# Performance work log

Measured on AMD Instinct MI355X. Metric: run time of the kernel, lower is better.

Reference implementation:

```python
import jax, jax.numpy as jnp
import numpy as np

N_NODES = 100000
N_EDGES = 1600000
NFEAT, NHID, NCLASS, NL = 128, 64, 40, 6


def setup_inputs() -> dict:
    key = jax.random.key(0)
    ks = jax.random.split(key, 12)
    x = jax.random.normal(ks[0], (N_NODES, NFEAT), dtype=jnp.float32)
    edge_row = jax.random.randint(ks[1], (N_EDGES,), 0, N_NODES)
    edge_col = jax.random.randint(ks[2], (N_EDGES,), 0, N_NODES)
    # positive values mimicking a degree-normalized adjacency
    edge_val = jax.random.uniform(ks[3], (N_EDGES,), dtype=jnp.float32) / 16.0
    s1 = 1.0 / np.sqrt(NFEAT)
    sh = 1.0 / np.sqrt(NHID)
    W1 = jax.random.uniform(ks[4], (NFEAT, NHID), minval=-s1, maxval=s1, dtype=jnp.float32)
    b1 = jax.random.uniform(ks[5], (NHID,), minval=-s1, maxval=s1, dtype=jnp.float32)
    Wm = jax.random.uniform(ks[6], (NL, NHID, NHID), minval=-sh, maxval=sh, dtype=jnp.float32)
    bm = jax.random.uniform(ks[7], (NL, NHID), minval=-sh, maxval=sh, dtype=jnp.float32)
    W2 = jax.random.uniform(ks[8], (NHID, NCLASS), minval=-sh, maxval=sh, dtype=jnp.float32)
    b2 = jax.random.uniform(ks[9], (NCLASS,), minval=-sh, maxval=sh, dtype=jnp.float32)
    return {"x": x, "edge_row": edge_row, "edge_col": edge_col, "edge_val": edge_val,
            "W1": W1, "b1": b1, "Wm": Wm, "bm": bm, "W2": W2, "b2": b2}


def _gconv(h, row, col, val, W, b):
    # GraphConvolution: support = h @ W ; out = spmm(adj, support) + b
    support = h @ W                       # [N, out]
    msgs = val[:, None] * support[col]    # [E, out] gather
    agg = jax.ops.segment_sum(msgs, row, num_segments=h.shape[0])  # scatter-add
    return agg + b


def reference(x, edge_row, edge_col, edge_val, W1, b1, Wm, bm, W2, b2):
    # gc1: relu (dropout is identity in eval mode)
    h1 = jax.nn.relu(_gconv(x, edge_row, edge_col, edge_val, W1, b1))
    # first middle layer (module index 2): relu, no residual
    h2 = jax.nn.relu(_gconv(h1, edge_row, edge_col, edge_val, Wm[0], bm[0]))
    prev2, prev = h1, h2
    # remaining middle layers: relu + residual to two layers back
    for k in range(1, NL):
        h = jax.nn.relu(_gconv(prev, edge_row, edge_col, edge_val, Wm[k], bm[k])) + prev2
        prev2, prev = prev, h
    out = _gconv(prev, edge_row, edge_col, edge_val, W2, b2)  # gc2, no relu
    return jax.nn.log_softmax(out, axis=1)
```

## Files before the change

kernel.cpp:

```cpp
#include <hip/hip_runtime.h>
#include <hip/hip_bf16.h>
#include <math.h>

#define N_NODES 100000
#define N_EDGES 1600000
#define NFEAT 128
#define NHID  64
#define NCLASS 40
#define NL 6

#define NBUK 256
#define RPB  391
#define EPP  (N_EDGES / NBUK)
#define EP_PAD 256
#define NTILES (N_NODES / 16)

typedef __attribute__((ext_vector_type(8))) short short8;
typedef __attribute__((ext_vector_type(8))) unsigned short ushort8v;
typedef __attribute__((ext_vector_type(4))) float floatx4;

__device__ __forceinline__ float bfbits(unsigned short u) {
  return __uint_as_float((unsigned int)u << 16);
}
__device__ __forceinline__ short f2bs(float f) {
  __hip_bfloat16 h = __float2bfloat16(f);
  return *reinterpret_cast<short*>(&h);
}

__global__ __launch_bounds__(1024) void p0_hist_k(const int* __restrict__ row,
                                                  int* __restrict__ h2d) {
  __shared__ int h[NBUK];
  const int i = blockIdx.x, t = threadIdx.x;
  if (t < NBUK) h[t] = 0;
  __syncthreads();
  const int e0 = i * EPP, e1 = e0 + EPP;
  for (int e = e0 + t; e < e1; e += 1024) atomicAdd(&h[row[e] / RPB], 1);
  __syncthreads();
  if (t < NBUK) h2d[i * NBUK + t] = h[t];
}

__global__ __launch_bounds__(256) void k1_scanb_k(int* __restrict__ h2d,
                                                  int* __restrict__ btot) {
  __shared__ int sd[256];
  const int b = blockIdx.x, t = threadIdx.x;
  int v = h2d[t * NBUK + b];
  sd[t] = v;
  __syncthreads();
  for (int off = 1; off < 256; off <<= 1) {
    int a = (t >= off) ? sd[t - off] : 0;
    __syncthreads();
    sd[t] += a;
    __syncthreads();
  }
  h2d[t * NBUK + b] = sd[t] - v;
  if (t == 255) btot[b] = sd[255];
}

__global__ __launch_bounds__(256) void k2_scanbase_k(const int* __restrict__ btot,
                                                     int* __restrict__ bbase,
                                                     int2* __restrict__ ep) {
  __shared__ int sd[256];
  const int t = threadIdx.x;
  int v = btot[t];
  sd[t] = v;
  __syncthreads();
  for (int off = 1; off < 256; off <<= 1) {
    int a = (t >= off) ? sd[t - off] : 0;
    __syncthreads();
    sd[t] += a;
    __syncthreads();
  }
  bbase[t] = sd[t] - v;
  if (t == 255) bbase[256] = sd[255];
  if (t < EP_PAD) ep[N_EDGES + t] = make_int2(0, 0);
}

__global__ __launch_bounds__(1024) void p2_part_k(
    const int* __restrict__ row, const int* __restrict__ col,
    const float* __restrict__ val, const int* __restrict__ h2d,
    const int* __restrict__ bbase, int2* __restrict__ pcv,
    unsigned short* __restrict__ plr) {
  __shared__ int cur[NBUK];
  const int i = blockIdx.x, t = threadIdx.x;
  if (t < NBUK) cur[t] = bbase[t] + h2d[i * NBUK + t];
  __syncthreads();
  const int e0 = i * EPP, e1 = e0 + EPP;
  for (int e = e0 + t; e < e1; e += 1024) {
    int r = row[e];
    int b = r / RPB;
    int p = atomicAdd(&cur[b], 1);
    pcv[p] = make_int2(col[e], __float_as_int(val[e]));
    plr[p] = (unsigned short)(r - b * RPB);
  }
}

__global__ __launch_bounds__(1024) void p3_fine_k(const int2* __restrict__ pcv,
                                                  const unsigned short* __restrict__ plr,
                                                  const int* __restrict__ bbase,
                                                  int* __restrict__ rp,
                                                  int2* __restrict__ ep) {
  __shared__ int cnt[RPB];
  __shared__ int cur[RPB];
  const int b = blockIdx.x, t = threadIdx.x;
  const int ebeg = bbase[b], eend = bbase[b + 1];
  const int r0 = b * RPB;
  const int nloc = min(RPB, N_NODES - r0);

  for (int i = t; i < RPB; i += 1024) cnt[i] = 0;
  __syncthreads();
  for (int j = ebeg + t; j < eend; j += 1024) atomicAdd(&cnt[plr[j]], 1);
  __syncthreads();

  if (t < 64) {
    const int base_ = t * 7;
    int v[7], s = 0;
#pragma unroll
    for (int k = 0; k < 7; ++k) {
      int idx = base_ + k;
      v[k] = (idx < RPB) ? cnt[idx] : 0;
      s += v[k];
    }
    int incl = s;
#pragma unroll
    for (int off = 1; off < 64; off <<= 1) {
      int y = __shfl_up(incl, off);
      if (t >= off) incl += y;
    }
    int run = incl - s;
#pragma unroll
    for (int k = 0; k < 7; ++k) {
      int idx = base_ + k;
      if (idx < RPB) cnt[idx] = run;
      run += v[k];
    }
  }
  __syncthreads();

  for (int i = t; i < nloc; i += 1024) {
    rp[r0 + i] = ebeg + cnt[i];
    cur[i] = cnt[i];
  }
  if (b == 0 && t == 0) rp[N_NODES] = N_EDGES;
  __syncthreads();

  for (int j = ebeg + t; j < eend; j += 1024) {
    int lr = plr[j];
    int p = atomicAdd(&cur[lr], 1);
    ep[ebeg + p] = pcv[j];
  }
}

__global__ __launch_bounds__(256) void gemm_l1(const float* __restrict__ X,
                                               const float* __restrict__ W,
                                               unsigned short* __restrict__ S) {
  const int lane = threadIdx.x & 63;
  const int quad = lane >> 4;
  const int m = lane & 15;

  short8 bf[4][4];
#pragma unroll
  for (int t = 0; t < 4; ++t)
#pragma unroll
    for (int h = 0; h < 4; ++h)
#pragma unroll
      for (int j = 0; j < 8; ++j)
        bf[t][h][j] = f2bs(W[(h * 32 + quad * 8 + j) * 64 + t * 16 + m]);

  const int wid = blockIdx.x * 4 + (threadIdx.x >> 6);
  for (int tile = wid; tile < NTILES; tile += gridDim.x * 4) {
    const int r0 = tile * 16;
    const float* xr = X + (size_t)(r0 + m) * 128;
    short8 af[4];
#pragma unroll
    for (int h = 0; h < 4; ++h) {
      const float* p = xr + h * 32 + quad * 8;
      float4 a = *(const float4*)p;
      float4 b = *(const float4*)(p + 4);
      af[h][0] = f2bs(a.x); af[h][1] = f2bs(a.y);
      af[h][2] = f2bs(a.z); af[h][3] = f2bs(a.w);
      af[h][4] = f2bs(b.x); af[h][5] = f2bs(b.y);
      af[h][6] = f2bs(b.z); af[h][7] = f2bs(b.w);
    }
#pragma unroll
    for (int t = 0; t < 4; ++t) {
      floatx4 acc = {0.0f, 0.0f, 0.0f, 0.0f};
#pragma unroll
      for (int h = 0; h < 4; ++h)
        acc = __builtin_amdgcn_mfma_f32_16x16x32_bf16(af[h], bf[t][h], acc, 0, 0, 0);
#pragma unroll
      for (int r = 0; r < 4; ++r)
        S[(size_t)(r0 + quad * 4 + r) * 64 + t * 16 + m] = (unsigned short)f2bs(acc[r]);
    }
  }
}

template <int COLS>
__global__ __launch_bounds__(256) void gemm_bf(const unsigned short* __restrict__ Hb,
                                               const float* __restrict__ W,
                                               unsigned short* __restrict__ S) {
  const int lane = threadIdx.x & 63;
  const int quad = lane >> 4;
  const int m = lane & 15;

  short8 bf[4][2];
#pragma unroll
  for (int t = 0; t < 4; ++t) {
    const int cc = t * 16 + m;
#pragma unroll
    for (int h = 0; h < 2; ++h)
#pragma unroll
      for (int j = 0; j < 8; ++j)
        bf[t][h][j] = (COLS == 64 || cc < COLS)
                          ? f2bs(W[(h * 32 + quad * 8 + j) * COLS + cc])
                          : (short)0;
  }

  const int wid = blockIdx.x * 4 + (threadIdx.x >> 6);
  for (int tile = wid; tile < NTILES; tile += gridDim.x * 4) {
    const int r0 = tile * 16;
    const unsigned short* hr = Hb + (size_t)(r0 + m) * 64 + quad * 8;
    short8 af0 = *(const short8*)hr;
    short8 af1 = *(const short8*)(hr + 32);
#pragma unroll
    for (int t = 0; t < 4; ++t) {
      floatx4 acc = {0.0f, 0.0f, 0.0f, 0.0f};
      acc = __builtin_amdgcn_mfma_f32_16x16x32_bf16(af0, bf[t][0], acc, 0, 0, 0);
      acc = __builtin_amdgcn_mfma_f32_16x16x32_bf16(af1, bf[t][1], acc, 0, 0, 0);
#pragma unroll
      for (int r = 0; r < 4; ++r)
        S[(size_t)(r0 + quad * 4 + r) * 64 + t * 16 + m] = (unsigned short)f2bs(acc[r]);
    }
  }
}

template <bool RES>
__global__ __launch_bounds__(256) void spmm8_k(
    const unsigned short* __restrict__ S, const int2* __restrict__ ep,
    const int* __restrict__ rp, const float* __restrict__ bias,
    unsigned short* __restrict__ Hbout) {
  const int lane = threadIdx.x & 63;
  const int og = lane >> 3;
  const int i8 = lane & 7;
  const int sg = og & 3;
  const bool isB = og >= 4;
  const int pair = blockIdx.x * 4 + (threadIdx.x >> 6);
  const int nodeA = pair * 2;
  const int sA = rp[nodeA], sB = rp[nodeA + 1], eB = rp[nodeA + 2];
  const int myNode = nodeA + (isB ? 1 : 0);
  const int myBeg = isB ? sB : sA;
  const int myEnd = isB ? eB : sB;
  const int iters = (max(sB - sA, eB - sB) + 7) >> 3;

  float a[8] = {0, 0, 0, 0, 0, 0, 0, 0};
  int e = myBeg + sg;
  int2 q0 = ep[e], q1 = ep[e + 4];
  for (int it = 0; it < iters; ++it) {
    int2 n0 = ep[e + 8], n1 = ep[e + 12];
    float v0 = (e < myEnd) ? __int_as_float(q0.y) : 0.0f;
    float v1 = (e + 4 < myEnd) ? __int_as_float(q1.y) : 0.0f;
    ushort8v s0 = *(const ushort8v*)(S + ((size_t)q0.x * 64 + i8 * 8));
    ushort8v s1 = *(const ushort8v*)(S + ((size_t)q1.x * 64 + i8 * 8));
#pragma unroll
    for (int j = 0; j < 8; ++j) a[j] = fmaf(v0, bfbits(s0[j]), a[j]);
#pragma unroll
    for (int j = 0; j < 8; ++j) a[j] = fmaf(v1, bfbits(s1[j]), a[j]);
    q0 = n0; q1 = n1; e += 8;
  }

#pragma unroll
  for (int j = 0; j < 8; ++j) {
    a[j] += __shfl_xor(a[j], 8);
    a[j] += __shfl_xor(a[j], 16);
  }

  if (sg == 0) {
    float4 b0 = ((const float4*)bias)[i8 * 2];
    float4 b1 = ((const float4*)bias)[i8 * 2 + 1];
    float h[8];
    h[0] = fmaxf(a[0] + b0.x, 0.0f); h[1] = fmaxf(a[1] + b0.y, 0.0f);
    h[2] = fmaxf(a[2] + b0.z, 0.0f); h[3] = fmaxf(a[3] + b0.w, 0.0f);
    h[4] = fmaxf(a[4] + b1.x, 0.0f); h[5] = fmaxf(a[5] + b1.y, 0.0f);
    h[6] = fmaxf(a[6] + b1.z, 0.0f); h[7] = fmaxf(a[7] + b1.w, 0.0f);
    if (RES) {
      ushort8v r = ((const ushort8v*)Hbout)[(size_t)myNode * 8 + i8];
#pragma unroll
      for (int j = 0; j < 8; ++j) h[j] += bfbits(r[j]);
    }
    ushort8v hb;
#pragma unroll
    for (int j = 0; j < 8; ++j) hb[j] = (unsigned short)f2bs(h[j]);
    ((ushort8v*)Hbout)[(size_t)myNode * 8 + i8] = hb;
  }
}

__global__ __launch_bounds__(256) void spmm_final_k(
    const unsigned short* __restrict__ S, const int2* __restrict__ ep,
    const int* __restrict__ rp, const float* __restrict__ b2,
    float* __restrict__ out) {
  const int lane = threadIdx.x & 63;
  const int og = lane >> 3;
  const int i8 = lane & 7;
  const int sg = og & 3;
  const bool isB = og >= 4;
  const int pair = blockIdx.x * 4 + (threadIdx.x >> 6);
  const int nodeA = pair * 2;
  const int sA = rp[nodeA], sB = rp[nodeA + 1], eB = rp[nodeA + 2];
  const int myNode = nodeA + (isB ? 1 : 0);
  const int myBeg = isB ? sB : sA;
  const int myEnd = isB ? eB : sB;
  const int iters = (max(sB - sA, eB - sB) + 7) >> 3;

  float a[8] = {0, 0, 0, 0, 0, 0, 0, 0};
  int e = myBeg + sg;
  int2 q0 = ep[e], q1 = ep[e + 4];
  for (int it = 0; it < iters; ++it) {
    int2 n0 = ep[e + 8], n1 = ep[e + 12];
    float v0 = (e < myEnd) ? __int_as_float(q0.y) : 0.0f;
    float v1 = (e + 4 < myEnd) ? __int_as_float(q1.y) : 0.0f;
    ushort8v s0 = *(const ushort8v*)(S + ((size_t)q0.x * 64 + i8 * 8));
    ushort8v s1 = *(const ushort8v*)(S + ((size_t)q1.x * 64 + i8 * 8));
#pragma unroll
    for (int j = 0; j < 8; ++j) a[j] = fmaf(v0, bfbits(s0[j]), a[j]);
#pragma unroll
    for (int j = 0; j < 8; ++j) a[j] = fmaf(v1, bfbits(s1[j]), a[j]);
    q0 = n0; q1 = n1; e += 8;
  }

#pragma unroll
  for (int j = 0; j < 8; ++j) {
    a[j] += __shfl_xor(a[j], 8);
    a[j] += __shfl_xor(a[j], 16);
  }

  const bool valid = (i8 < 5);
  float l[8];
  float mx = -INFINITY;
  if (valid) {
    float4 c0 = ((const float4*)b2)[i8 * 2];
    float4 c1 = ((const float4*)b2)[i8 * 2 + 1];
    l[0] = a[0] + c0.x; l[1] = a[1] + c0.y; l[2] = a[2] + c0.z; l[3] = a[3] + c0.w;
    l[4] = a[4] + c1.x; l[5] = a[5] + c1.y; l[6] = a[6] + c1.z; l[7] = a[7] + c1.w;
#pragma unroll
    for (int j = 0; j < 8; ++j) mx = fmaxf(mx, l[j]);
  }
#pragma unroll
  for (int off = 1; off < 8; off <<= 1) mx = fmaxf(mx, __shfl_xor(mx, off));
  float sum = 0.0f;
  if (valid) {
#pragma unroll
    for (int j = 0; j < 8; ++j) sum += expf(l[j] - mx);
  }
#pragma unroll
  for (int off = 1; off < 8; off <<= 1) sum += __shfl_xor(sum, off);

  if (sg == 0 && valid) {
    float lg = mx + logf(sum);
    ((float4*)out)[(size_t)myNode * 10 + i8 * 2] =
        make_float4(l[0] - lg, l[1] - lg, l[2] - lg, l[3] - lg);
    ((float4*)out)[(size_t)myNode * 10 + i8 * 2 + 1] =
        make_float4(l[4] - lg, l[5] - lg, l[6] - lg, l[7] - lg);
  }
}

extern "C" void kernel_launch(void* const* d_in, const int* in_sizes, int n_in,
                              void* d_out, int out_size, void* d_ws, size_t ws_size,
                              hipStream_t stream) {
  const float* x    = (const float*)d_in[0];
  const int*   erow = (const int*)d_in[1];
  const int*   ecol = (const int*)d_in[2];
  const float* eval = (const float*)d_in[3];
  const float* W1   = (const float*)d_in[4];
  const float* b1   = (const float*)d_in[5];
  const float* Wm   = (const float*)d_in[6];
  const float* bm   = (const float*)d_in[7];
  const float* W2   = (const float*)d_in[8];
  const float* b2   = (const float*)d_in[9];
  float* out = (float*)d_out;

  char* ws = (char*)d_ws;
  size_t off = 0;
  auto alloc = [&](size_t bytes) {
    void* p = ws + off;
    off = (off + bytes + 255) & ~(size_t)255;
    return p;
  };
  int*  rp    = (int*)alloc((N_NODES + 1) * sizeof(int));
  int*  h2d   = (int*)alloc((size_t)NBUK * NBUK * sizeof(int));
  int*  btot  = (int*)alloc(NBUK * sizeof(int));
  int*  bbase = (int*)alloc((NBUK + 1) * sizeof(int));
  int2* ep    = (int2*)alloc((size_t)(N_EDGES + EP_PAD) * sizeof(int2));
  char* U     = (char*)alloc((size_t)N_EDGES * sizeof(int2) +
                             (((size_t)N_EDGES * sizeof(unsigned short) + 255) & ~(size_t)255));
  int2* pcv = (int2*)U;
  unsigned short* plr = (unsigned short*)(U + (size_t)N_EDGES * sizeof(int2));
  unsigned short* S = (unsigned short*)U;
  unsigned short* B0 = (unsigned short*)alloc((size_t)N_NODES * 64 * sizeof(unsigned short));
  unsigned short* B1 = (unsigned short*)alloc((size_t)N_NODES * 64 * sizeof(unsigned short));

  const int SPMM_GRID = N_NODES / 8;
  const int GEMM_GRID = 512;

  p0_hist_k<<<NBUK, 1024, 0, stream>>>(erow, h2d);
  k1_scanb_k<<<NBUK, 256, 0, stream>>>(h2d, btot);
  k2_scanbase_k<<<1, 256, 0, stream>>>(btot, bbase, ep);
  p2_part_k<<<NBUK, 1024, 0, stream>>>(erow, ecol, eval, h2d, bbase, pcv, plr);
  p3_fine_k<<<NBUK, 1024, 0, stream>>>(pcv, plr, bbase, rp, ep);

  gemm_l1<<<GEMM_GRID, 256, 0, stream>>>(x, W1, S);
  spmm8_k<false><<<SPMM_GRID, 256, 0, stream>>>(S, ep, rp, b1, B0);

  gemm_bf<64><<<GEMM_GRID, 256, 0, stream>>>(B0, Wm, S);
  spmm8_k<false><<<SPMM_GRID, 256, 0, stream>>>(S, ep, rp, bm, B1);

  gemm_bf<64><<<GEMM_GRID, 256, 0, stream>>>(B1, Wm + 1 * 4096, S);
  spmm8_k<true><<<SPMM_GRID, 256, 0, stream>>>(S, ep, rp, bm + 1 * 64, B0);

  gemm_bf<64><<<GEMM_GRID, 256, 0, stream>>>(B0, Wm + 2 * 4096, S);
  spmm8_k<true><<<SPMM_GRID, 256, 0, stream>>>(S, ep, rp, bm + 2 * 64, B1);

  gemm_bf<64><<<GEMM_GRID, 256, 0, stream>>>(B1, Wm + 3 * 4096, S);
  spmm8_k<true><<<SPMM_GRID, 256, 0, stream>>>(S, ep, rp, bm + 3 * 64, B0);

  gemm_bf<64><<<GEMM_GRID, 256, 0, stream>>>(B0, Wm + 4 * 4096, S);
  spmm8_k<true><<<SPMM_GRID, 256, 0, stream>>>(S, ep, rp, bm + 4 * 64, B1);

  gemm_bf<64><<<GEMM_GRID, 256, 0, stream>>>(B1, Wm + 5 * 4096, S);
  spmm8_k<true><<<SPMM_GRID, 256, 0, stream>>>(S, ep, rp, bm + 5 * 64, B0);

  gemm_bf<40><<<GEMM_GRID, 256, 0, stream>>>(B0, W2, S);
  spmm_final_k<<<SPMM_GRID, 256, 0, stream>>>(S, ep, rp, b2, out);
}
```

Before: 511.6 us.

## Fuse next-layer dense GEMM into SpMM epilogue via shared-memory tile

Each SpMM block now aggregates 16 nodes with 8 waves, stages the resulting bf16 hidden rows in LDS, and wave 0 multiplies that tile by the next layer's weights with MFMA, writing the next support matrix directly. This removes the seven standalone gemm_bf launches and their re-read of the hidden activations from global memory. The cost is a block-wide barrier, with one wave doing the GEMM while the rest idle. A second S buffer is added so reads and writes ping-pong.

```diff
diff --git a/kernel.cpp b/kernel.cpp
--- a/kernel.cpp
+++ b/kernel.cpp
@@ -194,62 +194,46 @@
   }
 }
 
-template <int COLS>
-__global__ __launch_bounds__(256) void gemm_bf(const unsigned short* __restrict__ Hb,
-                                               const float* __restrict__ W,
-                                               unsigned short* __restrict__ S) {
-  const int lane = threadIdx.x & 63;
-  const int quad = lane >> 4;
-  const int m = lane & 15;
-
-  short8 bf[4][2];
-#pragma unroll
-  for (int t = 0; t < 4; ++t) {
-    const int cc = t * 16 + m;
-#pragma unroll
-    for (int h = 0; h < 2; ++h)
-#pragma unroll
-      for (int j = 0; j < 8; ++j)
-        bf[t][h][j] = (COLS == 64 || cc < COLS)
-                          ? f2bs(W[(h * 32 + quad * 8 + j) * COLS + cc])
-                          : (short)0;
-  }
-
-  const int wid = blockIdx.x * 4 + (threadIdx.x >> 6);
-  for (int tile = wid; tile < NTILES; tile += gridDim.x * 4) {
-    const int r0 = tile * 16;
-    const unsigned short* hr = Hb + (size_t)(r0 + m) * 64 + quad * 8;
-    short8 af0 = *(const short8*)hr;
-    short8 af1 = *(const short8*)(hr + 32);
-#pragma unroll
-    for (int t = 0; t < 4; ++t) {
-      floatx4 acc = {0.0f, 0.0f, 0.0f, 0.0f};
-      acc = __builtin_amdgcn_mfma_f32_16x16x32_bf16(af0, bf[t][0], acc, 0, 0, 0);
-      acc = __builtin_amdgcn_mfma_f32_16x16x32_bf16(af1, bf[t][1], acc, 0, 0, 0);
-#pragma unroll
-      for (int r = 0; r < 4; ++r)
-        S[(size_t)(r0 + quad * 4 + r) * 64 + t * 16 + m] = (unsigned short)f2bs(acc[r]);
-    }
-  }
-}
-
-template <bool RES>
-__global__ __launch_bounds__(256) void spmm8_k(
+template <bool RES, int COLS>
+__global__ __launch_bounds__(512) void spmm_fused_k(
     const unsigned short* __restrict__ S, const int2* __restrict__ ep,
     const int* __restrict__ rp, const float* __restrict__ bias,
-    unsigned short* __restrict__ Hbout) {
-  const int lane = threadIdx.x & 63;
+    unsigned short* __restrict__ Hb,
+    const float* __restrict__ Wn,
+    unsigned short* __restrict__ Sout) {
+  __shared__ alignas(16) unsigned short hl[16 * 72];
+
+  const int tid = threadIdx.x;
+  const int lane = tid & 63;
+  const int wv = tid >> 6;
   const int og = lane >> 3;
   const int i8 = lane & 7;
   const int sg = og & 3;
   const bool isB = og >= 4;
-  const int pair = blockIdx.x * 4 + (threadIdx.x >> 6);
-  const int nodeA = pair * 2;
+
+  const int blk0 = blockIdx.x * 16;
+  const int nodeA = blk0 + wv * 2;
   const int sA = rp[nodeA], sB = rp[nodeA + 1], eB = rp[nodeA + 2];
   const int myNode = nodeA + (isB ? 1 : 0);
   const int myBeg = isB ? sB : sA;
   const int myEnd = isB ? eB : sB;
   const int iters = (max(sB - sA, eB - sB) + 7) >> 3;
+
+  short8 bfrag[4][2];
+  if (wv == 0) {
+    const int quad = lane >> 4, m = lane & 15;
+#pragma unroll
+    for (int t = 0; t < 4; ++t) {
+      const int cc = t * 16 + m;
+#pragma unroll
+      for (int h = 0; h < 2; ++h)
+#pragma unroll
+        for (int j = 0; j < 8; ++j)
+          bfrag[t][h][j] = (COLS == 64 || cc < COLS)
+                               ? f2bs(Wn[(h * 32 + quad * 8 + j) * COLS + cc])
+                               : (short)0;
+    }
+  }
 
   float a[8] = {0, 0, 0, 0, 0, 0, 0, 0};
   int e = myBeg + sg;
@@ -282,14 +266,33 @@
     h[4] = fmaxf(a[4] + b1.x, 0.0f); h[5] = fmaxf(a[5] + b1.y, 0.0f);
     h[6] = fmaxf(a[6] + b1.z, 0.0f); h[7] = fmaxf(a[7] + b1.w, 0.0f);
     if (RES) {
-      ushort8v r = ((const ushort8v*)Hbout)[(size_t)myNode * 8 + i8];
+      ushort8v r = ((const ushort8v*)Hb)[(size_t)myNode * 8 + i8];
 #pragma unroll
       for (int j = 0; j < 8; ++j) h[j] += bfbits(r[j]);
     }
     ushort8v hb;
 #pragma unroll
     for (int j = 0; j < 8; ++j) hb[j] = (unsigned short)f2bs(h[j]);
-    ((ushort8v*)Hbout)[(size_t)myNode * 8 + i8] = hb;
+    ((ushort8v*)Hb)[(size_t)myNode * 8 + i8] = hb;
+    const int ln = myNode - blk0;
+    *(ushort8v*)&hl[ln * 72 + i8 * 8] = hb;
+  }
+  __syncthreads();
+
+  if (wv == 0) {
+    const int quad = lane >> 4, m = lane & 15;
+    short8 a0 = *(const short8*)&hl[m * 72 + quad * 8];
+    short8 a1 = *(const short8*)&hl[m * 72 + 32 + quad * 8];
+#pragma unroll
+    for (int t = 0; t < 4; ++t) {
+      floatx4 acc = {0.0f, 0.0f, 0.0f, 0.0f};
+      acc = __builtin_amdgcn_mfma_f32_16x16x32_bf16(a0, bfrag[t][0], acc, 0, 0, 0);
+      acc = __builtin_amdgcn_mfma_f32_16x16x32_bf16(a1, bfrag[t][1], acc, 0, 0, 0);
+#pragma unroll
+      for (int r = 0; r < 4; ++r)
+        Sout[(size_t)(blk0 + quad * 4 + r) * 64 + t * 16 + m] =
+            (unsigned short)f2bs(acc[r]);
+    }
   }
 }
 
@@ -393,11 +396,13 @@
                              (((size_t)N_EDGES * sizeof(unsigned short) + 255) & ~(size_t)255));
   int2* pcv = (int2*)U;
   unsigned short* plr = (unsigned short*)(U + (size_t)N_EDGES * sizeof(int2));
-  unsigned short* S = (unsigned short*)U;
+  unsigned short* Sa = (unsigned short*)U;
+  unsigned short* Sb = (unsigned short*)alloc((size_t)N_NODES * 64 * sizeof(unsigned short));
   unsigned short* B0 = (unsigned short*)alloc((size_t)N_NODES * 64 * sizeof(unsigned short));
   unsigned short* B1 = (unsigned short*)alloc((size_t)N_NODES * 64 * sizeof(unsigned short));
 
-  const int SPMM_GRID = N_NODES / 8;
+  const int FUSE_GRID = N_NODES / 16;
+  const int FINAL_GRID = N_NODES / 8;
   const int GEMM_GRID = 512;
 
   p0_hist_k<<<NBUK, 1024, 0, stream>>>(erow, h2d);
@@ -406,27 +411,15 @@
   p2_part_k<<<NBUK, 1024, 0, stream>>>(erow, ecol, eval, h2d, bbase, pcv, plr);
   p3_fine_k<<<NBUK, 1024, 0, stream>>>(pcv, plr, bbase, rp, ep);
 
-  gemm_l1<<<GEMM_GRID, 256, 0, stream>>>(x, W1, S);
-  spmm8_k<false><<<SPMM_GRID, 256, 0, stream>>>(S, ep, rp, b1, B0);
-
-  gemm_bf<64><<<GEMM_GRID, 256, 0, stream>>>(B0, Wm, S);
-  spmm8_k<false><<<SPMM_GRID, 256, 0, stream>>>(S, ep, rp, bm, B1);
-
-  gemm_bf<64><<<GEMM_GRID, 256, 0, stream>>>(B1, Wm + 1 * 4096, S);
-  spmm8_k<true><<<SPMM_GRID, 256, 0, stream>>>(S, ep, rp, bm + 1 * 64, B0);
-
-  gemm_bf<64><<<GEMM_GRID, 256, 0, stream>>>(B0, Wm + 2 * 4096, S);
-  spmm8_k<true><<<SPMM_GRID, 256, 0, stream>>>(S, ep, rp, bm + 2 * 64, B1);
-
-  gemm_bf<64><<<GEMM_GRID, 256, 0, stream>>>(B1, Wm + 3 * 4096, S);
-  spmm8_k<true><<<SPMM_GRID, 256, 0, stream>>>(S, ep, rp, bm + 3 * 64, B0);
-
-  gemm_bf<64><<<GEMM_GRID, 256, 0, stream>>>(B0, Wm + 4 * 4096, S);
-  spmm8_k<true><<<SPMM_GRID, 256, 0, stream>>>(S, ep, rp, bm + 4 * 64, B1);
-
-  gemm_bf<64><<<GEMM_GRID, 256, 0, stream>>>(B1, Wm + 5 * 4096, S);
-  spmm8_k<true><<<SPMM_GRID, 256, 0, stream>>>(S, ep, rp, bm + 5 * 64, B0);
-
-  gemm_bf<40><<<GEMM_GRID, 256, 0, stream>>>(B0, W2, S);
-  spmm_final_k<<<SPMM_GRID, 256, 0, stream>>>(S, ep, rp, b2, out);
-}
+  gemm_l1<<<GEMM_GRID, 256, 0, stream>>>(x, W1, Sa);
+
+  spmm_fused_k<false, 64><<<FUSE_GRID, 512, 0, stream>>>(Sa, ep, rp, b1, B0, Wm, Sb);
+  spmm_fused_k<false, 64><<<FUSE_GRID, 512, 0, stream>>>(Sb, ep, rp, bm, B1, Wm + 4096, Sa);
+  spmm_fused_k<true, 64><<<FUSE_GRID, 512, 0, stream>>>(Sa, ep, rp, bm + 64, B0, Wm + 2 * 4096, Sb);
+  spmm_fused_k<true, 64><<<FUSE_GRID, 512, 0, stream>>>(Sb, ep, rp, bm + 128, B1, Wm + 3 * 4096, Sa);
+  spmm_fused_k<true, 64><<<FUSE_GRID, 512, 0, stream>>>(Sa, ep, rp, bm + 192, B0, Wm + 4 * 4096, Sb);
+  spmm_fused_k<true, 64><<<FUSE_GRID, 512, 0, stream>>>(Sb, ep, rp, bm + 256, B1, Wm + 5 * 4096, Sa);
+  spmm_fused_k<true, 40><<<FUSE_GRID, 512, 0, stream>>>(Sa, ep, rp, bm + 320, B0, W2, Sb);
+
+  spmm_final_k<<<FINAL_GRID, 256, 0, stream>>>(Sb, ep, rp, b2, out);
+}
```

Result: slower. 591.9 us (+15.7%).
